# Kernel tuning notes

Measured on AMD Instinct MI355X. Metric: run time of the kernel, lower is better.

## Reference

```python
import jax, jax.numpy as jnp
import numpy as np

N_SEG = 1024  # segments per image (ids are contiguous in [0, N_SEG) after reindex_batch_segments)


def setup_inputs() -> dict:
    key = jax.random.key(0)
    k1, k2, k3, k4 = jax.random.split(key, 4)
    B, C, Hf, Wf = 4, 256, 16, 16
    H, W = 512, 512
    F_out = 192
    features = jax.random.normal(k1, (B, C, Hf, Wf), dtype=jnp.float32)
    w_conv = jax.random.normal(k2, (F_out, C), dtype=jnp.float32) / np.sqrt(C)
    b_conv = jax.random.normal(k3, (F_out,), dtype=jnp.float32) * 0.01
    segment = jax.random.randint(k4, (B, H, W), 0, N_SEG, dtype=jnp.int32)
    return {"features": features, "w_conv": w_conv, "b_conv": b_conv, "segment": segment}


def reference(features, w_conv, b_conv, segment):
    # features: (B, C, Hf, Wf) backbone output; segment: (B, H, W) int ids in [0, N_SEG)
    B, C, Hf, Wf = features.shape
    _, H, W = segment.shape
    # F.interpolate(..., mode='bilinear', align_corners=False) == half-pixel linear resize
    up = jax.image.resize(features, (B, C, H, W), method="bilinear")
    pix = up.transpose(0, 2, 3, 1).reshape(B * H * W, C)  # (B*H*W, C)
    # offset per-image segment ids into a global id space: id + b * N_SEG
    seg = (segment.reshape(B, H * W) + (jnp.arange(B, dtype=segment.dtype) * N_SEG)[:, None]).reshape(-1)
    sums = jax.ops.segment_sum(pix, seg, num_segments=B * N_SEG)              # (B*N, C)
    cnt = jax.ops.segment_sum(jnp.ones((B * H * W,), pix.dtype), seg, num_segments=B * N_SEG)
    mean = sums / jnp.maximum(cnt, 1.0)[:, None]
    feats = mean.reshape(B, N_SEG, C)                                          # (B, N, C)
    # last_conv: 1x1 Conv1d (C -> F_out) applied on (B, C, N), then permute(0, 2, 1)
    out = jnp.einsum("bnc,fc->bnf", feats, w_conv) + b_conv                    # (B, N, F_out)
    return out, segment
```

## Files before the change

### kernel.cpp

```cpp
#include <hip/hip_runtime.h>
#include <hip/hip_bf16.h>

constexpr int B_   = 4;
constexpr int C_   = 256;
constexpr int HF   = 16;
constexpr int WF   = 16;
constexpr int HH   = 512;
constexpr int WW   = 512;
constexpr int NSEG = 1024;
constexpr int FOUT = 192;
constexpr int NCELL = HF * WF;
constexpr int CB    = B_ * NCELL;
constexpr int GPB   = 48;

struct PS { float Fs[32][65]; float Ws[64][33]; };

union CellSMem {
    struct { unsigned lbin[NSEG]; unsigned wr[64]; unsigned wc[64]; } c;
    PS p;
};

__device__ void gemm_P_body(int gp, const float* __restrict__ feat,
                            const float* __restrict__ w, float* __restrict__ P,
                            PS& sm) {
    int ni = gp % 3;
    int mi = (gp / 3) & 3;
    int b  = gp / 12;
    const float* Fb = feat + (size_t)b * C_ * NCELL;

    int tid = threadIdx.x;
    int tx = tid & 15, ty = tid >> 4;
    float acc[4][4] = {};

    for (int k0 = 0; k0 < C_; k0 += 32) {
        #pragma unroll
        for (int l = 0; l < 2; ++l) {
            int li = tid * 2 + l;
            int kk = li >> 4;
            int m4 = (li & 15) * 4;
            float4 vf = *reinterpret_cast<const float4*>(&Fb[(size_t)(k0 + kk) * NCELL + mi * 64 + m4]);
            sm.Fs[kk][m4 + 0] = vf.x; sm.Fs[kk][m4 + 1] = vf.y;
            sm.Fs[kk][m4 + 2] = vf.z; sm.Fs[kk][m4 + 3] = vf.w;
            int row = li >> 3;
            int kq  = (li & 7) * 4;
            float4 vw = *reinterpret_cast<const float4*>(&w[(size_t)(ni * 64 + row) * C_ + k0 + kq]);
            sm.Ws[row][kq + 0] = vw.x; sm.Ws[row][kq + 1] = vw.y;
            sm.Ws[row][kq + 2] = vw.z; sm.Ws[row][kq + 3] = vw.w;
        }
        __syncthreads();
        #pragma unroll
        for (int kk = 0; kk < 32; ++kk) {
            float ar[4], wr[4];
            #pragma unroll
            for (int i = 0; i < 4; ++i) ar[i] = sm.Fs[kk][ty * 4 + i];
            #pragma unroll
            for (int j = 0; j < 4; ++j) wr[j] = sm.Ws[tx * 4 + j][kk];
            #pragma unroll
            for (int i = 0; i < 4; ++i)
                #pragma unroll
                for (int j = 0; j < 4; ++j) acc[i][j] += ar[i] * wr[j];
        }
        __syncthreads();
    }

    #pragma unroll
    for (int i = 0; i < 4; ++i)
        #pragma unroll
        for (int j = 0; j < 4; ++j)
            P[(size_t)b * NCELL * FOUT + (size_t)(mi * 64 + ty * 4 + i) * FOUT + ni * 64 + tx * 4 + j] = acc[i][j];
}

__global__ __launch_bounds__(256) void k_cell(const int* __restrict__ seg,
                                              float* __restrict__ segout,
                                              float* __restrict__ AT,
                                              const float* __restrict__ feat,
                                              const float* __restrict__ w,
                                              float* __restrict__ P) {
    __shared__ CellSMem sm;
    int blk = blockIdx.x;
    if (blk >= CB) { gemm_P_body(blk - CB, feat, w, P, sm.p); return; }

    int tid  = threadIdx.x;
    int b    = blk >> 8;
    int cell = blk & 255;
    int cy = cell >> 4, cx = cell & 15;

    {
        const int4* sv = reinterpret_cast<const int4*>(seg + (size_t)blk * 1024);
        float4* ov = reinterpret_cast<float4*>(segout + (size_t)blk * 1024);
        int4 v = sv[tid];
        ov[tid] = make_float4((float)v.x, (float)v.y, (float)v.z, (float)v.w);
    }

    #pragma unroll
    for (int j = 0; j < 4; ++j) sm.c.lbin[tid * 4 + j] = 0u;
    int ys = 32 * cy - 16, xs = 32 * cx - 16;
    if (tid < 128) {
        int r  = tid & 63;
        int cc = (tid < 64) ? cy : cx;
        int v  = ((tid < 64) ? ys : xs) + r;
        unsigned wgt = 0u;
        if (v >= 0 && v < 512) {
            int twov = 2 * v - 31;
            int num  = ((twov % 64) + 64) % 64;
            int iv   = (twov - num) >> 6;
            int v0 = max(iv, 0), v1 = min(iv + 1, 15);
            wgt = (unsigned)((v0 == cc ? 64 - num : 0) + (v1 == cc ? num : 0));
        }
        if (tid < 64) sm.c.wr[r] = wgt; else sm.c.wc[r] = wgt;
    }
    __syncthreads();

    int rr = tid >> 4;
    int cg = (tid & 15) * 4;
    unsigned wc0 = sm.c.wc[cg + 0], wc1 = sm.c.wc[cg + 1];
    unsigned wc2 = sm.c.wc[cg + 2], wc3 = sm.c.wc[cg + 3];

    const int* srow = seg + (size_t)b * (HH * WW);
    #pragma unroll
    for (int rnd = 0; rnd < 4; ++rnd) {
        int r = rnd * 16 + rr;
        int y = ys + r;
        int x0 = xs + cg;
        if (y >= 0 && y < HH && x0 >= 0 && x0 + 3 < WW) {
            unsigned wy = sm.c.wr[r];
            if (wy) {
                int4 v = *reinterpret_cast<const int4*>(srow + (size_t)y * WW + x0);
                atomicAdd(&sm.c.lbin[v.x], wy * wc0);
                atomicAdd(&sm.c.lbin[v.y], wy * wc1);
                atomicAdd(&sm.c.lbin[v.z], wy * wc2);
                atomicAdd(&sm.c.lbin[v.w], wy * wc3);
            }
        }
    }
    __syncthreads();

    float4* dst = reinterpret_cast<float4*>(AT + ((size_t)(b * NCELL + cell)) * NSEG);
    constexpr float SCL = 1.0f / 4096.0f;
    dst[tid] = make_float4(sm.c.lbin[tid * 4 + 0] * SCL, sm.c.lbin[tid * 4 + 1] * SCL,
                           sm.c.lbin[tid * 4 + 2] * SCL, sm.c.lbin[tid * 4 + 3] * SCL);
}

__global__ __launch_bounds__(256) void k_gemm_out(const float* __restrict__ AT,
                                                  const float* __restrict__ P,
                                                  const float* __restrict__ bias,
                                                  float* __restrict__ out) {
    int ft = blockIdx.x % 3;
    int st = blockIdx.x / 3;
    int b  = st >> 4;
    int s0 = (st & 15) * 64;

    const float* ATb = AT + (size_t)b * NCELL * NSEG;
    const float* Pb  = P  + (size_t)b * NCELL * FOUT;

    __shared__ float As[32][65];
    __shared__ float Ps[32][65];

    int tid = threadIdx.x;
    int tx = tid & 15, ty = tid >> 4;
    float acc[4][4] = {};
    float cnt[4] = {};

    for (int k0 = 0; k0 < NCELL; k0 += 32) {
        #pragma unroll
        for (int l = 0; l < 2; ++l) {
            int li = tid * 2 + l;
            int kk = li >> 4;
            int e4 = (li & 15) * 4;
            float4 va = *reinterpret_cast<const float4*>(&ATb[(size_t)(k0 + kk) * NSEG + s0 + e4]);
            As[kk][e4 + 0] = va.x; As[kk][e4 + 1] = va.y;
            As[kk][e4 + 2] = va.z; As[kk][e4 + 3] = va.w;
            float4 vp = *reinterpret_cast<const float4*>(&Pb[(size_t)(k0 + kk) * FOUT + ft * 64 + e4]);
            Ps[kk][e4 + 0] = vp.x; Ps[kk][e4 + 1] = vp.y;
            Ps[kk][e4 + 2] = vp.z; Ps[kk][e4 + 3] = vp.w;
        }
        __syncthreads();
        #pragma unroll
        for (int kk = 0; kk < 32; ++kk) {
            float ar[4], wr[4];
            #pragma unroll
            for (int i = 0; i < 4; ++i) { ar[i] = As[kk][ty * 4 + i]; cnt[i] += ar[i]; }
            #pragma unroll
            for (int j = 0; j < 4; ++j) wr[j] = Ps[kk][tx * 4 + j];
            #pragma unroll
            for (int i = 0; i < 4; ++i)
                #pragma unroll
                for (int j = 0; j < 4; ++j) acc[i][j] += ar[i] * wr[j];
        }
        __syncthreads();
    }

    #pragma unroll
    for (int i = 0; i < 4; ++i) {
        int row = st * 64 + ty * 4 + i;
        float rinv = 1.0f / fmaxf(cnt[i], 1.0f);
        #pragma unroll
        for (int j = 0; j < 4; ++j) {
            int f = ft * 64 + tx * 4 + j;
            out[(size_t)row * FOUT + f] = acc[i][j] * rinv + bias[f];
        }
    }
}

extern "C" void kernel_launch(void* const* d_in, const int* in_sizes, int n_in,
                              void* d_out, int out_size, void* d_ws, size_t ws_size,
                              hipStream_t stream) {
    const float* feat = (const float*)d_in[0];
    const float* w    = (const float*)d_in[1];
    const float* bias = (const float*)d_in[2];
    const int*   seg  = (const int*)d_in[3];

    float* out    = (float*)d_out;
    float* segout = out + (size_t)B_ * NSEG * FOUT;

    char* wsb = (char*)d_ws;
    float* AT = (float*)wsb;
    float* P  = (float*)(wsb + (5u << 20));

    k_cell    <<<CB + GPB, 256, 0, stream>>>(seg, segout, AT, feat, w, P);
    k_gemm_out<<<(B_ * NSEG / 64) * (FOUT / 64), 256, 0, stream>>>(AT, P, bias, out);
}
```

Before: 49.03 us.

## Restructure cell histogram loads, schedule GEMM-P blocks first, halve output GEMM tile rows

The cell kernel now has each thread load 16 contiguous segment ids (one int4 x4) from a clamped row window and compute its row weight inline. This replaces the four guarded rounds of 4-wide loads, lets the segment-copy store overlap with the loads, and drops the wr shared table. The small GEMM-P blocks now take the low block indices so they are scheduled first. The output GEMM tile shrinks from 64 to 32 segments per block, doubling the grid to fill more CUs at the cost of more P-tile reloads. Clamped out-of-range rows and columns rely on their weights being zero so they contribute nothing.

```diff
diff --git a/kernel.cpp b/kernel.cpp
--- a/kernel.cpp
+++ b/kernel.cpp
@@ -16,7 +16,7 @@
 struct PS { float Fs[32][65]; float Ws[64][33]; };
 
 union CellSMem {
-    struct { unsigned lbin[NSEG]; unsigned wr[64]; unsigned wc[64]; } c;
+    struct { unsigned lbin[NSEG]; unsigned wc[64]; } c;
     PS p;
 };
 
@@ -70,6 +70,15 @@
             P[(size_t)b * NCELL * FOUT + (size_t)(mi * 64 + ty * 4 + i) * FOUT + ni * 64 + tx * 4 + j] = acc[i][j];
 }
 
+__device__ __forceinline__ unsigned tapw(int v, int cc) {
+    if (v < 0 || v >= 512) return 0u;
+    int twov = 2 * v - 31;
+    int num  = ((twov % 64) + 64) % 64;
+    int iv   = (twov - num) >> 6;
+    int v0 = max(iv, 0), v1 = min(iv + 1, 15);
+    return (unsigned)((v0 == cc ? 64 - num : 0) + (v1 == cc ? num : 0));
+}
+
 __global__ __launch_bounds__(256) void k_cell(const int* __restrict__ seg,
                                               float* __restrict__ segout,
                                               float* __restrict__ AT,
@@ -78,61 +87,58 @@
                                               float* __restrict__ P) {
     __shared__ CellSMem sm;
     int blk = blockIdx.x;
-    if (blk >= CB) { gemm_P_body(blk - CB, feat, w, P, sm.p); return; }
-
+    if (blk < GPB) { gemm_P_body(blk, feat, w, P, sm.p); return; }
+
+    int cb   = blk - GPB;
     int tid  = threadIdx.x;
-    int b    = blk >> 8;
-    int cell = blk & 255;
+    int b    = cb >> 8;
+    int cell = cb & 255;
     int cy = cell >> 4, cx = cell & 15;
-
-    {
-        const int4* sv = reinterpret_cast<const int4*>(seg + (size_t)blk * 1024);
-        float4* ov = reinterpret_cast<float4*>(segout + (size_t)blk * 1024);
-        int4 v = sv[tid];
-        ov[tid] = make_float4((float)v.x, (float)v.y, (float)v.z, (float)v.w);
-    }
+    int ys = 32 * cy - 16, xs = 32 * cx - 16;
+
+    const int4* sv = reinterpret_cast<const int4*>(seg + (size_t)cb * 1024);
+    float4*     ov = reinterpret_cast<float4*>(segout + (size_t)cb * 1024);
+    int4 pv = sv[tid];
 
     #pragma unroll
     for (int j = 0; j < 4; ++j) sm.c.lbin[tid * 4 + j] = 0u;
-    int ys = 32 * cy - 16, xs = 32 * cx - 16;
-    if (tid < 128) {
-        int r  = tid & 63;
-        int cc = (tid < 64) ? cy : cx;
-        int v  = ((tid < 64) ? ys : xs) + r;
-        unsigned wgt = 0u;
-        if (v >= 0 && v < 512) {
-            int twov = 2 * v - 31;
-            int num  = ((twov % 64) + 64) % 64;
-            int iv   = (twov - num) >> 6;
-            int v0 = max(iv, 0), v1 = min(iv + 1, 15);
-            wgt = (unsigned)((v0 == cc ? 64 - num : 0) + (v1 == cc ? num : 0));
-        }
-        if (tid < 64) sm.c.wr[r] = wgt; else sm.c.wc[r] = wgt;
-    }
+    if (tid < 64) sm.c.wc[tid] = tapw(xs + tid, cx);
+
+    int r  = tid >> 2;
+    int y  = ys + r;
+    unsigned wrv = tapw(y, cy);
+    int yc = min(max(y, 0), HH - 1);
+    int cg = (tid & 3) * 16;
+    int x0 = xs + cg;
+    int xc = min(max(x0, 0), WW - 16);
+
+    const int4* lrow = reinterpret_cast<const int4*>(seg + (size_t)b * (HH * WW) + (size_t)yc * WW + xc);
+    int4 v0 = lrow[0], v1 = lrow[1], v2 = lrow[2], v3 = lrow[3];
+
+    ov[tid] = make_float4((float)pv.x, (float)pv.y, (float)pv.z, (float)pv.w);
     __syncthreads();
 
-    int rr = tid >> 4;
-    int cg = (tid & 15) * 4;
-    unsigned wc0 = sm.c.wc[cg + 0], wc1 = sm.c.wc[cg + 1];
-    unsigned wc2 = sm.c.wc[cg + 2], wc3 = sm.c.wc[cg + 3];
-
-    const int* srow = seg + (size_t)b * (HH * WW);
-    #pragma unroll
-    for (int rnd = 0; rnd < 4; ++rnd) {
-        int r = rnd * 16 + rr;
-        int y = ys + r;
-        int x0 = xs + cg;
-        if (y >= 0 && y < HH && x0 >= 0 && x0 + 3 < WW) {
-            unsigned wy = sm.c.wr[r];
-            if (wy) {
-                int4 v = *reinterpret_cast<const int4*>(srow + (size_t)y * WW + x0);
-                atomicAdd(&sm.c.lbin[v.x], wy * wc0);
-                atomicAdd(&sm.c.lbin[v.y], wy * wc1);
-                atomicAdd(&sm.c.lbin[v.z], wy * wc2);
-                atomicAdd(&sm.c.lbin[v.w], wy * wc3);
-            }
-        }
-    }
+    uint4 wa = *reinterpret_cast<const uint4*>(&sm.c.wc[cg + 0]);
+    uint4 wb = *reinterpret_cast<const uint4*>(&sm.c.wc[cg + 4]);
+    uint4 wcv = *reinterpret_cast<const uint4*>(&sm.c.wc[cg + 8]);
+    uint4 wd = *reinterpret_cast<const uint4*>(&sm.c.wc[cg + 12]);
+
+    atomicAdd(&sm.c.lbin[v0.x], wrv * wa.x);
+    atomicAdd(&sm.c.lbin[v0.y], wrv * wa.y);
+    atomicAdd(&sm.c.lbin[v0.z], wrv * wa.z);
+    atomicAdd(&sm.c.lbin[v0.w], wrv * wa.w);
+    atomicAdd(&sm.c.lbin[v1.x], wrv * wb.x);
+    atomicAdd(&sm.c.lbin[v1.y], wrv * wb.y);
+    atomicAdd(&sm.c.lbin[v1.z], wrv * wb.z);
+    atomicAdd(&sm.c.lbin[v1.w], wrv * wb.w);
+    atomicAdd(&sm.c.lbin[v2.x], wrv * wcv.x);
+    atomicAdd(&sm.c.lbin[v2.y], wrv * wcv.y);
+    atomicAdd(&sm.c.lbin[v2.z], wrv * wcv.z);
+    atomicAdd(&sm.c.lbin[v2.w], wrv * wcv.w);
+    atomicAdd(&sm.c.lbin[v3.x], wrv * wd.x);
+    atomicAdd(&sm.c.lbin[v3.y], wrv * wd.y);
+    atomicAdd(&sm.c.lbin[v3.z], wrv * wd.z);
+    atomicAdd(&sm.c.lbin[v3.w], wrv * wd.w);
     __syncthreads();
 
     float4* dst = reinterpret_cast<float4*>(AT + ((size_t)(b * NCELL + cell)) * NSEG);
@@ -147,43 +153,45 @@
                                                   float* __restrict__ out) {
     int ft = blockIdx.x % 3;
     int st = blockIdx.x / 3;
-    int b  = st >> 4;
-    int s0 = (st & 15) * 64;
+    int b  = st >> 5;
+    int s0 = (st & 31) * 32;
 
     const float* ATb = AT + (size_t)b * NCELL * NSEG;
     const float* Pb  = P  + (size_t)b * NCELL * FOUT;
 
-    __shared__ float As[32][65];
+    __shared__ float As[32][33];
     __shared__ float Ps[32][65];
 
     int tid = threadIdx.x;
     int tx = tid & 15, ty = tid >> 4;
-    float acc[4][4] = {};
-    float cnt[4] = {};
+    float acc[2][4] = {};
+    float cnt[2] = {};
 
     for (int k0 = 0; k0 < NCELL; k0 += 32) {
-        #pragma unroll
-        for (int l = 0; l < 2; ++l) {
-            int li = tid * 2 + l;
-            int kk = li >> 4;
-            int e4 = (li & 15) * 4;
+        {
+            int kk = tid >> 3, e4 = (tid & 7) * 4;
             float4 va = *reinterpret_cast<const float4*>(&ATb[(size_t)(k0 + kk) * NSEG + s0 + e4]);
             As[kk][e4 + 0] = va.x; As[kk][e4 + 1] = va.y;
             As[kk][e4 + 2] = va.z; As[kk][e4 + 3] = va.w;
-            float4 vp = *reinterpret_cast<const float4*>(&Pb[(size_t)(k0 + kk) * FOUT + ft * 64 + e4]);
-            Ps[kk][e4 + 0] = vp.x; Ps[kk][e4 + 1] = vp.y;
-            Ps[kk][e4 + 2] = vp.z; Ps[kk][e4 + 3] = vp.w;
+            #pragma unroll
+            for (int l = 0; l < 2; ++l) {
+                int li = tid * 2 + l;
+                int kp = li >> 4, e = (li & 15) * 4;
+                float4 vp = *reinterpret_cast<const float4*>(&Pb[(size_t)(k0 + kp) * FOUT + ft * 64 + e]);
+                Ps[kp][e + 0] = vp.x; Ps[kp][e + 1] = vp.y;
+                Ps[kp][e + 2] = vp.z; Ps[kp][e + 3] = vp.w;
+            }
         }
         __syncthreads();
         #pragma unroll
         for (int kk = 0; kk < 32; ++kk) {
-            float ar[4], wr[4];
-            #pragma unroll
-            for (int i = 0; i < 4; ++i) { ar[i] = As[kk][ty * 4 + i]; cnt[i] += ar[i]; }
+            float ar[2], wr[4];
+            #pragma unroll
+            for (int i = 0; i < 2; ++i) { ar[i] = As[kk][ty * 2 + i]; cnt[i] += ar[i]; }
             #pragma unroll
             for (int j = 0; j < 4; ++j) wr[j] = Ps[kk][tx * 4 + j];
             #pragma unroll
-            for (int i = 0; i < 4; ++i)
+            for (int i = 0; i < 2; ++i)
                 #pragma unroll
                 for (int j = 0; j < 4; ++j) acc[i][j] += ar[i] * wr[j];
         }
@@ -191,8 +199,8 @@
     }
 
     #pragma unroll
-    for (int i = 0; i < 4; ++i) {
-        int row = st * 64 + ty * 4 + i;
+    for (int i = 0; i < 2; ++i) {
+        int row = b * NSEG + s0 + ty * 2 + i;
         float rinv = 1.0f / fmaxf(cnt[i], 1.0f);
         #pragma unroll
         for (int j = 0; j < 4; ++j) {
@@ -217,6 +225,6 @@
     float* AT = (float*)wsb;
     float* P  = (float*)(wsb + (5u << 20));
 
-    k_cell    <<<CB + GPB, 256, 0, stream>>>(seg, segout, AT, feat, w, P);
-    k_gemm_out<<<(B_ * NSEG / 64) * (FOUT / 64), 256, 0, stream>>>(AT, P, bias, out);
-}
+    k_cell    <<<GPB + CB, 256, 0, stream>>>(seg, segout, AT, feat, w, P);
+    k_gemm_out<<<(B_ * NSEG / 32) * (FOUT / 64), 256, 0, stream>>>(AT, P, bias, out);
+}
```

Result: no change. 48.54 us, median of 2 (-1.0%).
